# Performance work log

Hardware: AMD Instinct MI355X
Metric: run time of the kernel (lower is better)

## Reference

```python
import jax, jax.numpy as jnp
import numpy as np

DIM = 32
HID = 128          # edge-MLP hidden width
N = 8192           # total nodes
E = 131072         # total edges
B = 64             # number of graphs
NUM_MP = 3
S2S_STEPS = 3


def setup_inputs() -> dict:
    key = jax.random.key(0)
    ks = jax.random.split(key, 24)
    g = lambda k, shape, s=0.05: jax.random.normal(k, shape, dtype=jnp.float32) * s

    inp = {
        "x": jax.random.normal(ks[0], (N, 1), dtype=jnp.float32),
        "edge_attr": jax.random.uniform(ks[1], (E, 2), dtype=jnp.float32),
        # params
        "lin0_w": g(ks[2], (1, DIM)), "lin0_b": g(ks[3], (DIM,)),
        "enn_w1": g(ks[4], (2, HID)), "enn_b1": g(ks[5], (HID,)),
        "enn_w2": g(ks[6], (HID, DIM * DIM)), "enn_b2": g(ks[7], (DIM * DIM,)),
        "root_w": g(ks[8], (DIM, DIM)), "conv_b": g(ks[9], (DIM,)),
        # GRU (gates ordered r,z,n as in torch)
        "gru_wih": g(ks[10], (DIM, 3 * DIM)), "gru_whh": g(ks[11], (DIM, 3 * DIM)),
        "gru_bih": g(ks[12], (3 * DIM,)), "gru_bhh": g(ks[13], (3 * DIM,)),
        # Set2Set LSTM: input 2*DIM, hidden DIM (gates ordered i,f,g,o as in torch)
        "s2s_wih": g(ks[14], (2 * DIM, 4 * DIM)), "s2s_whh": g(ks[15], (DIM, 4 * DIM)),
        "s2s_bih": g(ks[16], (4 * DIM,)), "s2s_bhh": g(ks[17], (4 * DIM,)),
        "lin1_w": g(ks[18], (2 * DIM, DIM)), "lin1_b": g(ks[19], (DIM,)),
        "lin2_w": g(ks[20], (DIM, 1)), "lin2_b": g(ks[21], (1,)),
        # int args
        "edge_index": jax.random.randint(ks[22], (2, E), 0, N, dtype=jnp.int32),
        "batch": jnp.sort(jax.random.randint(ks[23], (N,), 0, B, dtype=jnp.int32)),
    }
    return inp


def _forward(x, edge_attr, lin0_w, lin0_b, enn_w1, enn_b1, enn_w2, enn_b2,
             root_w, conv_b, gru_wih, gru_whh, gru_bih, gru_bhh,
             s2s_wih, s2s_whh, s2s_bih, s2s_bhh, lin1_w, lin1_b, lin2_w, lin2_b,
             edge_index, batch):
    src, dst = edge_index[0], edge_index[1]

    out = jax.nn.relu(x @ lin0_w + lin0_b)          # [N, DIM]
    h = out                                          # GRU hidden state

    # edge-conditioned weights (constant across MP layers -> hoisted)
    ew = jax.nn.relu(edge_attr @ enn_w1 + enn_b1) @ enn_w2 + enn_b2
    W = ew.reshape(E, DIM, DIM)                      # [E, in, out]

    deg = jnp.maximum(jax.ops.segment_sum(jnp.ones((E,), jnp.float32), dst,
                                          num_segments=N), 1.0)[:, None]

    for _ in range(NUM_MP):
        # NNConv: gather -> per-edge small matmul -> scatter-mean, + root + bias
        msg = jnp.einsum('ed,edo->eo', out[src], W)  # [E, DIM]
        agg = jax.ops.segment_sum(msg, dst, num_segments=N) / deg
        m = jax.nn.relu(agg + out @ root_w + conv_b)
        # GRU cell (single step)
        gi = m @ gru_wih + gru_bih
        gh = h @ gru_whh + gru_bhh
        ir, iz, in_ = jnp.split(gi, 3, axis=-1)
        hr, hz, hn = jnp.split(gh, 3, axis=-1)
        r = jax.nn.sigmoid(ir + hr)
        z = jax.nn.sigmoid(iz + hz)
        n = jnp.tanh(in_ + r * hn)
        h = (1.0 - z) * n + z * h
        out = h

    # Set2Set pooling
    qh = jnp.zeros((B, DIM), jnp.float32)
    qc = jnp.zeros((B, DIM), jnp.float32)
    q_star = jnp.zeros((B, 2 * DIM), jnp.float32)
    for _ in range(S2S_STEPS):
        gates = q_star @ s2s_wih + s2s_bih + qh @ s2s_whh + s2s_bhh
        i_, f_, g_, o_ = jnp.split(gates, 4, axis=-1)
        qc = jax.nn.sigmoid(f_) * qc + jax.nn.sigmoid(i_) * jnp.tanh(g_)
        qh = jax.nn.sigmoid(o_) * jnp.tanh(qc)       # [B, DIM]
        e = jnp.sum(out * qh[batch], axis=-1)        # [N] attention logits
        emax = jax.ops.segment_max(e, batch, num_segments=B)
        a = jnp.exp(e - emax[batch])
        a = a / jax.ops.segment_sum(a, batch, num_segments=B)[batch]
        r_read = jax.ops.segment_sum(a[:, None] * out, batch, num_segments=B)
        q_star = jnp.concatenate([qh, r_read], axis=-1)  # [B, 2*DIM]

    y = jax.nn.relu(q_star @ lin1_w + lin1_b) @ lin2_w + lin2_b
    return y.reshape(-1)                              # [B]


def reference(x, edge_attr, lin0_w, lin0_b, enn_w1, enn_b1, enn_w2, enn_b2,
              root_w, conv_b, gru_wih, gru_whh, gru_bih, gru_bhh,
              s2s_wih, s2s_whh, s2s_bih, s2s_bhh, lin1_w, lin1_b, lin2_w, lin2_b,
              edge_index, batch):
    return _forward(x, edge_attr, lin0_w, lin0_b, enn_w1, enn_b1, enn_w2, enn_b2,
                    root_w, conv_b, gru_wih, gru_whh, gru_bih, gru_bhh,
                    s2s_wih, s2s_whh, s2s_bih, s2s_bhh, lin1_w, lin1_b, lin2_w,
                    lin2_b, edge_index, batch)
```

## Files before the change

kernel.cpp:

```cpp
#include <hip/hip_runtime.h>

#define N_NODES 8192
#define N_EDGES 131072
#define NGRAPH  64
#define DIM     32
#define HID     128
#define SROW    34

__device__ __forceinline__ float sigmoidf_(float x) { return 1.0f / (1.0f + expf(-x)); }

__global__ void init_nodes_kernel(const float* __restrict__ x,
                                  const float* __restrict__ w,
                                  const float* __restrict__ b,
                                  float* __restrict__ out) {
  int idx = blockIdx.x * 256 + threadIdx.x;
  if (idx >= N_NODES * DIM) return;
  int n = idx >> 5, d = idx & 31;
  out[idx] = fmaxf(fmaf(x[n], w[d], b[d]), 0.0f);
}

__global__ void hist_kernel(const int* __restrict__ dst, int* __restrict__ counts) {
  int e = blockIdx.x * 256 + threadIdx.x;
  if (e < N_EDGES) atomicAdd(&counts[dst[e]], 1);
}

__global__ void scan_kernel(const int* __restrict__ counts,
                            int* __restrict__ offsets,
                            float* __restrict__ deg_inv) {
  __shared__ int sm[1024];
  int t = threadIdx.x;
  int base = t * 8;
  int loc[8];
  int s = 0;
#pragma unroll
  for (int i = 0; i < 8; ++i) { loc[i] = s; s += counts[base + i]; }
  sm[t] = s;
  __syncthreads();
  for (int off = 1; off < 1024; off <<= 1) {
    int v = (t >= off) ? sm[t - off] : 0;
    __syncthreads();
    sm[t] += v;
    __syncthreads();
  }
  int excl = (t > 0) ? sm[t - 1] : 0;
#pragma unroll
  for (int i = 0; i < 8; ++i) {
    offsets[base + i] = excl + loc[i];
    int c = counts[base + i];
    deg_inv[base + i] = 1.0f / (float)(c > 0 ? c : 1);
  }
  if (t == 1023) offsets[N_NODES] = sm[1023];
}

__global__ void scatter_kernel(const int* __restrict__ ei,
                               const float* __restrict__ ea,
                               const int* __restrict__ offsets,
                               int* __restrict__ cursor,
                               int* __restrict__ csr_src,
                               float2* __restrict__ csr_ea) {
  int e = blockIdx.x * 256 + threadIdx.x;
  if (e >= N_EDGES) return;
  int d = ei[N_EDGES + e];
  int pos = atomicAdd(&cursor[d], 1);
  int slot = offsets[d] + pos;
  csr_src[slot] = ei[e];
  csr_ea[slot] = make_float2(ea[2 * e], ea[2 * e + 1]);
}

__global__ void gstart_kernel(const int* __restrict__ batch, int* __restrict__ gstart) {
  int n = blockIdx.x * 256 + threadIdx.x;
  if (n >= N_NODES) return;
  int b = batch[n];
  if (n == 0) {
    for (int g = 0; g <= b; ++g) gstart[g] = 0;
  } else {
    int bp = batch[n - 1];
    for (int g = bp + 1; g <= b; ++g) gstart[g] = n;
  }
  if (n == N_NODES - 1) {
    for (int g = b + 1; g <= NGRAPH; ++g) gstart[g] = N_NODES;
  }
}

template <int G, int C>
__global__ __launch_bounds__(256) void mp_kernel(
    const float* __restrict__ out_cur, float* __restrict__ out_nxt,
    const int* __restrict__ offsets, const float* __restrict__ deg_inv,
    const int* __restrict__ csr_src, const float2* __restrict__ csr_ea,
    const float* __restrict__ w1, const float* __restrict__ b1,
    const float* __restrict__ w2, const float* __restrict__ b2,
    const float* __restrict__ root_w, const float* __restrict__ conv_b,
    const float* __restrict__ gwih, const float* __restrict__ gwhh,
    const float* __restrict__ gbih, const float* __restrict__ gbhh) {
  __shared__ float S[G * HID * SROW];
  __shared__ float hidb[C * HID];
  __shared__ float osrcb[C * DIM];
  __shared__ float Ob[G * DIM];
  __shared__ float aggb[G * DIM];
  __shared__ float mb[G * DIM];
  __shared__ float hb[G * DIM];
  __shared__ int offs[G + 1];
  __shared__ float dinvb[G];

  const int t = threadIdx.x;
  const int node0 = blockIdx.x * G;

  if (t <= G) offs[t] = offsets[min(node0 + t, N_NODES)];
  if (t < G) dinvb[t] = deg_inv[min(node0 + t, N_NODES - 1)];

  const int kg = t >> 3, dg = t & 7;
  const int k0 = kg * 4, d0 = dg * 4;
  const int ec = t / (256 / C);
  const int sub = t % (256 / C);
  __syncthreads();

  for (int g = 0; g < G; ++g) {
    float acc[4][4];
#pragma unroll
    for (int i = 0; i < 4; ++i)
#pragma unroll
      for (int j = 0; j < 4; ++j) acc[i][j] = 0.0f;
    float oacc = 0.0f;
    const int base = offs[g], end = offs[g + 1];
    for (int c0 = base; c0 < end; c0 += C) {
      const int cnt = min(C, end - c0);
      __syncthreads();
      if (ec < cnt) {
        const int slot = c0 + ec;
        const float2 eav = csr_ea[slot];
        const int sidx = csr_src[slot];
#pragma unroll
        for (int i = 0; i < HID / (256 / C); ++i) {
          const int k = sub * (HID / (256 / C)) + i;
          float v = fmaf(eav.y, w1[HID + k], fmaf(eav.x, w1[k], b1[k]));
          hidb[ec * HID + k] = fmaxf(v, 0.0f);
        }
        const float2 ov = *(const float2*)(out_cur + sidx * DIM + sub * 2);
        *(float2*)(osrcb + ec * DIM + sub * 2) = ov;
      }
      __syncthreads();
      for (int e = 0; e < cnt; ++e) {
        const float4 hv = *(const float4*)(hidb + e * HID + k0);
        const float4 ov = *(const float4*)(osrcb + e * DIM + d0);
        acc[0][0] = fmaf(hv.x, ov.x, acc[0][0]);
        acc[0][1] = fmaf(hv.x, ov.y, acc[0][1]);
        acc[0][2] = fmaf(hv.x, ov.z, acc[0][2]);
        acc[0][3] = fmaf(hv.x, ov.w, acc[0][3]);
        acc[1][0] = fmaf(hv.y, ov.x, acc[1][0]);
        acc[1][1] = fmaf(hv.y, ov.y, acc[1][1]);
        acc[1][2] = fmaf(hv.y, ov.z, acc[1][2]);
        acc[1][3] = fmaf(hv.y, ov.w, acc[1][3]);
        acc[2][0] = fmaf(hv.z, ov.x, acc[2][0]);
        acc[2][1] = fmaf(hv.z, ov.y, acc[2][1]);
        acc[2][2] = fmaf(hv.z, ov.z, acc[2][2]);
        acc[2][3] = fmaf(hv.z, ov.w, acc[2][3]);
        acc[3][0] = fmaf(hv.w, ov.x, acc[3][0]);
        acc[3][1] = fmaf(hv.w, ov.y, acc[3][1]);
        acc[3][2] = fmaf(hv.w, ov.z, acc[3][2]);
        acc[3][3] = fmaf(hv.w, ov.w, acc[3][3]);
        if (t < DIM) oacc += osrcb[e * DIM + t];
      }
    }
    float* Sg = S + g * HID * SROW;
#pragma unroll
    for (int i = 0; i < 4; ++i) {
      *(float2*)(Sg + (k0 + i) * SROW + d0) = make_float2(acc[i][0], acc[i][1]);
      *(float2*)(Sg + (k0 + i) * SROW + d0 + 2) = make_float2(acc[i][2], acc[i][3]);
    }
    if (t < DIM) Ob[g * DIM + t] = oacc;
  }
  __syncthreads();

  {
    const int ks = t >> 3, og = t & 7;
    const int o0 = og * 4;
    float a4[G][4];
#pragma unroll
    for (int g = 0; g < G; ++g)
#pragma unroll
      for (int j = 0; j < 4; ++j) a4[g][j] = 0.0f;
#pragma unroll
    for (int i = 0; i < 4; ++i) {
      const int k = ks * 4 + i;
      const float* w2k = w2 + k * (DIM * DIM);
#pragma unroll
      for (int dv = 0; dv < 8; ++dv) {
        const float4 wq0 = *(const float4*)(w2k + (dv * 4 + 0) * DIM + o0);
        const float4 wq1 = *(const float4*)(w2k + (dv * 4 + 1) * DIM + o0);
        const float4 wq2 = *(const float4*)(w2k + (dv * 4 + 2) * DIM + o0);
        const float4 wq3 = *(const float4*)(w2k + (dv * 4 + 3) * DIM + o0);
#pragma unroll
        for (int g = 0; g < G; ++g) {
          const float* Srow = S + g * HID * SROW + k * SROW + dv * 4;
          const float2 sa = *(const float2*)(Srow);
          const float2 sb = *(const float2*)(Srow + 2);
          a4[g][0] = fmaf(sa.x, wq0.x, fmaf(sa.y, wq1.x, fmaf(sb.x, wq2.x, fmaf(sb.y, wq3.x, a4[g][0]))));
          a4[g][1] = fmaf(sa.x, wq0.y, fmaf(sa.y, wq1.y, fmaf(sb.x, wq2.y, fmaf(sb.y, wq3.y, a4[g][1]))));
          a4[g][2] = fmaf(sa.x, wq0.z, fmaf(sa.y, wq1.z, fmaf(sb.x, wq2.z, fmaf(sb.y, wq3.z, a4[g][2]))));
          a4[g][3] = fmaf(sa.x, wq0.w, fmaf(sa.y, wq1.w, fmaf(sb.x, wq2.w, fmaf(sb.y, wq3.w, a4[g][3]))));
        }
      }
    }
    __syncthreads();
#pragma unroll
    for (int g = 0; g < G; ++g)
#pragma unroll
      for (int j = 0; j < 4; ++j) S[(g * 4 + j) * 256 + t] = a4[g][j];
  }
  __syncthreads();

  if (t < G * DIM) {
    const int g = t >> 5, o = t & 31;
    const int og = o >> 2, j = o & 3;
    float sum = 0.0f;
    for (int ks = 0; ks < 32; ++ks) sum += S[(g * 4 + j) * 256 + ks * 8 + og];
    float ob = 0.0f;
#pragma unroll
    for (int d = 0; d < DIM; ++d) ob = fmaf(Ob[g * DIM + d], b2[d * DIM + o], ob);
    aggb[t] = (sum + ob) * dinvb[g];
  }
  if (t < G * DIM) {
    const int g = t >> 5, o = t & 31;
    const int node = node0 + g;
    hb[t] = (node < N_NODES) ? out_cur[node * DIM + o] : 0.0f;
  }
  __syncthreads();
  if (t < G * DIM) {
    const int g = t >> 5, o = t & 31;
    float rt = conv_b[o];
#pragma unroll
    for (int d = 0; d < DIM; ++d) rt = fmaf(hb[g * DIM + d], root_w[d * DIM + o], rt);
    mb[t] = fmaxf(aggb[t] + rt, 0.0f);
  }
  __syncthreads();
  if (t < G * DIM) {
    const int g = t >> 5, o = t & 31;
    const int node = node0 + g;
    if (node < N_NODES) {
      float gi[3], gh[3];
#pragma unroll
      for (int jj = 0; jj < 3; ++jj) {
        float si = gbih[jj * DIM + o], sh = gbhh[jj * DIM + o];
#pragma unroll
        for (int d = 0; d < DIM; ++d) {
          si = fmaf(mb[g * DIM + d], gwih[d * 3 * DIM + jj * DIM + o], si);
          sh = fmaf(hb[g * DIM + d], gwhh[d * 3 * DIM + jj * DIM + o], sh);
        }
        gi[jj] = si;
        gh[jj] = sh;
      }
      const float r = sigmoidf_(gi[0] + gh[0]);
      const float z = sigmoidf_(gi[1] + gh[1]);
      const float nn = tanhf(fmaf(r, gh[2], gi[2]));
      out_nxt[node * DIM + o] = (1.0f - z) * nn + z * hb[t];
    }
  }
}

__global__ __launch_bounds__(256) void s2s_kernel(
    const float* __restrict__ outf, const int* __restrict__ gstart,
    const float* __restrict__ wih, const float* __restrict__ whh,
    const float* __restrict__ bih, const float* __restrict__ bhh,
    const float* __restrict__ l1w, const float* __restrict__ l1b,
    const float* __restrict__ l2w, const float* __restrict__ l2b,
    float* __restrict__ y) {
  __shared__ float qh[DIM], qc[DIM], qstar[2 * DIM], gates[4 * DIM];
  __shared__ float wsum[4], wmax[4], wr[4][DIM];
  const int b = blockIdx.x, t = threadIdx.x;
  const int gs = gstart[b], ge = gstart[b + 1];
  const int w = t >> 6, lane = t & 63;
  if (t < DIM) { qh[t] = 0.0f; qc[t] = 0.0f; }
  if (t < 2 * DIM) qstar[t] = 0.0f;
  __syncthreads();
  for (int step = 0; step < 3; ++step) {
    if (t < 4 * DIM) {
      float gv = bih[t] + bhh[t];
      for (int i = 0; i < 2 * DIM; ++i) gv = fmaf(qstar[i], wih[i * 4 * DIM + t], gv);
      for (int i = 0; i < DIM; ++i) gv = fmaf(qh[i], whh[i * 4 * DIM + t], gv);
      gates[t] = gv;
    }
    __syncthreads();
    if (t < DIM) {
      const float ig = sigmoidf_(gates[t]);
      const float fg = sigmoidf_(gates[DIM + t]);
      const float gg = tanhf(gates[2 * DIM + t]);
      const float og = sigmoidf_(gates[3 * DIM + t]);
      const float c = fmaf(fg, qc[t], ig * gg);
      qc[t] = c;
      qh[t] = og * tanhf(c);
    }
    __syncthreads();
    float lmax = -INFINITY;
    for (int n = gs + t; n < ge; n += 256) {
      const float* orow = outf + n * DIM;
      float e = 0.0f;
#pragma unroll
      for (int d = 0; d < DIM; ++d) e = fmaf(orow[d], qh[d], e);
      lmax = fmaxf(lmax, e);
    }
#pragma unroll
    for (int off = 32; off > 0; off >>= 1) lmax = fmaxf(lmax, __shfl_xor(lmax, off));
    if (lane == 0) wmax[w] = lmax;
    __syncthreads();
    const float gmax = fmaxf(fmaxf(wmax[0], wmax[1]), fmaxf(wmax[2], wmax[3]));
    float rl[DIM];
#pragma unroll
    for (int d = 0; d < DIM; ++d) rl[d] = 0.0f;
    float lsum = 0.0f;
    for (int n = gs + t; n < ge; n += 256) {
      const float* orow = outf + n * DIM;
      float e = 0.0f;
#pragma unroll
      for (int d = 0; d < DIM; ++d) e = fmaf(orow[d], qh[d], e);
      const float a = expf(e - gmax);
      lsum += a;
#pragma unroll
      for (int d = 0; d < DIM; ++d) rl[d] = fmaf(a, orow[d], rl[d]);
    }
#pragma unroll
    for (int off = 32; off > 0; off >>= 1) {
      lsum += __shfl_xor(lsum, off);
#pragma unroll
      for (int d = 0; d < DIM; ++d) rl[d] += __shfl_xor(rl[d], off);
    }
    __syncthreads();
    if (lane == 0) {
      wsum[w] = lsum;
#pragma unroll
      for (int d = 0; d < DIM; ++d) wr[w][d] = rl[d];
    }
    __syncthreads();
    if (t < DIM) {
      const float stot = wsum[0] + wsum[1] + wsum[2] + wsum[3];
      const float rv = wr[0][t] + wr[1][t] + wr[2][t] + wr[3][t];
      qstar[t] = qh[t];
      qstar[DIM + t] = (stot > 0.0f) ? rv / stot : 0.0f;
    }
    __syncthreads();
  }
  if (t < DIM) {
    float u = l1b[t];
    for (int i = 0; i < 2 * DIM; ++i) u = fmaf(qstar[i], l1w[i * DIM + t], u);
    u = fmaxf(u, 0.0f);
    float v = u * l2w[t];
#pragma unroll
    for (int off = 16; off > 0; off >>= 1) v += __shfl_xor(v, off);
    if (t == 0) y[b] = v + l2b[0];
  }
}

extern "C" void kernel_launch(void* const* d_in, const int* in_sizes, int n_in,
                              void* d_out, int out_size, void* d_ws, size_t ws_size,
                              hipStream_t stream) {
  const float* x        = (const float*)d_in[0];
  const float* ea       = (const float*)d_in[1];
  const float* lin0_w   = (const float*)d_in[2];
  const float* lin0_b   = (const float*)d_in[3];
  const float* enn_w1   = (const float*)d_in[4];
  const float* enn_b1   = (const float*)d_in[5];
  const float* enn_w2   = (const float*)d_in[6];
  const float* enn_b2   = (const float*)d_in[7];
  const float* root_w   = (const float*)d_in[8];
  const float* conv_b   = (const float*)d_in[9];
  const float* gru_wih  = (const float*)d_in[10];
  const float* gru_whh  = (const float*)d_in[11];
  const float* gru_bih  = (const float*)d_in[12];
  const float* gru_bhh  = (const float*)d_in[13];
  const float* s2s_wih  = (const float*)d_in[14];
  const float* s2s_whh  = (const float*)d_in[15];
  const float* s2s_bih  = (const float*)d_in[16];
  const float* s2s_bhh  = (const float*)d_in[17];
  const float* lin1_w   = (const float*)d_in[18];
  const float* lin1_b   = (const float*)d_in[19];
  const float* lin2_w   = (const float*)d_in[20];
  const float* lin2_b   = (const float*)d_in[21];
  const int*   ei       = (const int*)d_in[22];
  const int*   batch    = (const int*)d_in[23];
  float* y = (float*)d_out;

  char* p = (char*)d_ws;
  auto alloc = [&](size_t bytes) -> void* {
    void* r = (void*)p;
    p += (bytes + 255) & ~(size_t)255;
    return r;
  };
  float*  out_a   = (float*)alloc(N_NODES * DIM * 4);
  float*  out_b   = (float*)alloc(N_NODES * DIM * 4);
  int*    counts  = (int*)alloc(N_NODES * 4);
  int*    offsets = (int*)alloc((N_NODES + 1) * 4);
  int*    cursor  = (int*)alloc(N_NODES * 4);
  int*    csr_src = (int*)alloc(N_EDGES * 4);
  float2* csr_ea  = (float2*)alloc(N_EDGES * 8);
  float*  deg_inv = (float*)alloc(N_NODES * 4);
  int*    gstart  = (int*)alloc((NGRAPH + 1) * 4);
  (void)ws_size; (void)n_in; (void)in_sizes; (void)out_size;

  hipMemsetAsync(counts, 0, N_NODES * 4, stream);
  hipMemsetAsync(cursor, 0, N_NODES * 4, stream);

  init_nodes_kernel<<<(N_NODES * DIM) / 256, 256, 0, stream>>>(x, lin0_w, lin0_b, out_a);
  hist_kernel<<<N_EDGES / 256, 256, 0, stream>>>(ei + N_EDGES, counts);
  scan_kernel<<<1, 1024, 0, stream>>>(counts, offsets, deg_inv);
  scatter_kernel<<<N_EDGES / 256, 256, 0, stream>>>(ei, ea, offsets, cursor, csr_src, csr_ea);
  gstart_kernel<<<N_NODES / 256, 256, 0, stream>>>(batch, gstart);

  constexpr int G = 3, C = 16;
  const int mp_blocks = (N_NODES + G - 1) / G;
  mp_kernel<G, C><<<mp_blocks, 256, 0, stream>>>(
      out_a, out_b, offsets, deg_inv, csr_src, csr_ea, enn_w1, enn_b1, enn_w2, enn_b2,
      root_w, conv_b, gru_wih, gru_whh, gru_bih, gru_bhh);
  mp_kernel<G, C><<<mp_blocks, 256, 0, stream>>>(
      out_b, out_a, offsets, deg_inv, csr_src, csr_ea, enn_w1, enn_b1, enn_w2, enn_b2,
      root_w, conv_b, gru_wih, gru_whh, gru_bih, gru_bhh);
  mp_kernel<G, C><<<mp_blocks, 256, 0, stream>>>(
      out_a, out_b, offsets, deg_inv, csr_src, csr_ea, enn_w1, enn_b1, enn_w2, enn_b2,
      root_w, conv_b, gru_wih, gru_whh, gru_bih, gru_bhh);

  s2s_kernel<<<NGRAPH, 256, 0, stream>>>(out_b, gstart, s2s_wih, s2s_whh, s2s_bih, s2s_bhh,
                                         lin1_w, lin1_b, lin2_w, lin2_b, y);
}
```

Before: 501.6 us.

## Split message passing into build, contract, and epilogue kernels via global S buffer

Replaces the fused per-layer message-passing kernel with three kernels. The first builds per-node S = sum(hidden ⊗ x_src) matrices (4096 floats per node) in global memory. The second contracts S against enn_w2 as a 64-node-tiled GEMM with 16 K-slices of partial sums. The third reduces the partials and applies bias, root weight, ReLU and the GRU update. The aim is to amortise w2 loads across 64 nodes instead of 3, at the cost of writing and reading a 128 MB S buffer and 16 MB of partials per layer. It falls back to the old fused kernel when the workspace is too small.

```diff
diff --git a/kernel.cpp b/kernel.cpp
--- a/kernel.cpp
+++ b/kernel.cpp
@@ -5,6 +5,7 @@
 #define NGRAPH  64
 #define DIM     32
 #define HID     128
+#define SKD     4096
 #define SROW    34
 
 __device__ __forceinline__ float sigmoidf_(float x) { return 1.0f / (1.0f + expf(-x)); }
@@ -80,6 +81,219 @@
   if (n == N_NODES - 1) {
     for (int g = b + 1; g <= NGRAPH; ++g) gstart[g] = N_NODES;
   }
+}
+
+__global__ __launch_bounds__(256) void build_s_kernel(
+    const float* __restrict__ out_cur, const int* __restrict__ offsets,
+    const int* __restrict__ csr_src, const float2* __restrict__ csr_ea,
+    const float* __restrict__ w1, const float* __restrict__ b1,
+    float* __restrict__ S, float* __restrict__ O) {
+  constexpr int C = 16;
+  __shared__ float hidb[C * HID];
+  __shared__ float osrcb[C * DIM];
+  __shared__ int offs[5];
+  const int t = threadIdx.x;
+  const int node0 = blockIdx.x * 4;
+  if (t <= 4) offs[t] = offsets[node0 + t];
+  const int k0 = (t >> 3) * 4, d0 = (t & 7) * 4;
+  const int ec = t >> 4;
+  const int sub = t & 15;
+  float acc[4][4][4];
+#pragma unroll
+  for (int g = 0; g < 4; ++g)
+#pragma unroll
+    for (int i = 0; i < 4; ++i)
+#pragma unroll
+      for (int j = 0; j < 4; ++j) acc[g][i][j] = 0.0f;
+  float oacc[4] = {0.0f, 0.0f, 0.0f, 0.0f};
+  __syncthreads();
+#pragma unroll
+  for (int g = 0; g < 4; ++g) {
+    const int base = offs[g], end = offs[g + 1];
+    for (int c0 = base; c0 < end; c0 += C) {
+      const int cnt = min(C, end - c0);
+      __syncthreads();
+      if (ec < cnt) {
+        const int slot = c0 + ec;
+        const float2 eav = csr_ea[slot];
+        const int sidx = csr_src[slot];
+#pragma unroll
+        for (int i = 0; i < 8; ++i) {
+          const int k = sub * 8 + i;
+          hidb[ec * HID + k] =
+              fmaxf(fmaf(eav.y, w1[HID + k], fmaf(eav.x, w1[k], b1[k])), 0.0f);
+        }
+        *(float2*)(osrcb + ec * DIM + sub * 2) =
+            *(const float2*)(out_cur + sidx * DIM + sub * 2);
+      }
+      __syncthreads();
+      for (int e = 0; e < cnt; ++e) {
+        const float4 hv = *(const float4*)(hidb + e * HID + k0);
+        const float4 ov = *(const float4*)(osrcb + e * DIM + d0);
+        acc[g][0][0] = fmaf(hv.x, ov.x, acc[g][0][0]);
+        acc[g][0][1] = fmaf(hv.x, ov.y, acc[g][0][1]);
+        acc[g][0][2] = fmaf(hv.x, ov.z, acc[g][0][2]);
+        acc[g][0][3] = fmaf(hv.x, ov.w, acc[g][0][3]);
+        acc[g][1][0] = fmaf(hv.y, ov.x, acc[g][1][0]);
+        acc[g][1][1] = fmaf(hv.y, ov.y, acc[g][1][1]);
+        acc[g][1][2] = fmaf(hv.y, ov.z, acc[g][1][2]);
+        acc[g][1][3] = fmaf(hv.y, ov.w, acc[g][1][3]);
+        acc[g][2][0] = fmaf(hv.z, ov.x, acc[g][2][0]);
+        acc[g][2][1] = fmaf(hv.z, ov.y, acc[g][2][1]);
+        acc[g][2][2] = fmaf(hv.z, ov.z, acc[g][2][2]);
+        acc[g][2][3] = fmaf(hv.z, ov.w, acc[g][2][3]);
+        acc[g][3][0] = fmaf(hv.w, ov.x, acc[g][3][0]);
+        acc[g][3][1] = fmaf(hv.w, ov.y, acc[g][3][1]);
+        acc[g][3][2] = fmaf(hv.w, ov.z, acc[g][3][2]);
+        acc[g][3][3] = fmaf(hv.w, ov.w, acc[g][3][3]);
+        if (t < DIM) oacc[g] += osrcb[e * DIM + t];
+      }
+    }
+  }
+#pragma unroll
+  for (int g = 0; g < 4; ++g) {
+    const int node = node0 + g;
+    float* Sp = S + node * SKD + k0 * DIM + d0;
+#pragma unroll
+    for (int i = 0; i < 4; ++i)
+      *(float4*)(Sp + i * DIM) =
+          make_float4(acc[g][i][0], acc[g][i][1], acc[g][i][2], acc[g][i][3]);
+    if (t < DIM) O[node * DIM + t] = oacc[g];
+  }
+}
+
+#define SBPAD 68
+__global__ __launch_bounds__(256) void contract_kernel(
+    const float* __restrict__ S, const float* __restrict__ w2,
+    float* __restrict__ partial) {
+  __shared__ float sb[64 * SBPAD];
+  const int t = threadIdx.x;
+  const int nb = blockIdx.x >> 2;
+  const int kqb = blockIdx.x & 3;
+  const int node0 = nb * 64;
+  const int kbase = kqb * 1024;
+  const int w = t >> 6;
+  const int lane = t & 63;
+  const int ng = (lane >> 3) & 7;
+  const int og = lane & 7;
+  const int o0 = og * 4;
+  float acc[8][4];
+#pragma unroll
+  for (int i = 0; i < 8; ++i)
+#pragma unroll
+    for (int j = 0; j < 4; ++j) acc[i][j] = 0.0f;
+
+  const int ld_node = t >> 2;
+  const int ld_kds = (t & 3) * 16;
+
+  for (int c = 0; c < 16; ++c) {
+    __syncthreads();
+    const float* gsrc = S + (size_t)(node0 + ld_node) * SKD + kbase + c * 64 + ld_kds;
+#pragma unroll
+    for (int i = 0; i < 4; ++i) {
+      const float4 v = *(const float4*)(gsrc + i * 4);
+      const int kl = ld_kds + i * 4;
+      sb[(kl + 0) * SBPAD + ld_node] = v.x;
+      sb[(kl + 1) * SBPAD + ld_node] = v.y;
+      sb[(kl + 2) * SBPAD + ld_node] = v.z;
+      sb[(kl + 3) * SBPAD + ld_node] = v.w;
+    }
+    __syncthreads();
+#pragma unroll
+    for (int k4 = 0; k4 < 4; ++k4) {
+#pragma unroll
+      for (int kk = 0; kk < 4; ++kk) {
+        const int kdl = w * 16 + k4 * 4 + kk;
+        const int kd = kbase + c * 64 + kdl;
+        const float4 wv = *(const float4*)(w2 + (size_t)kd * 32 + o0);
+        const float4 sa = *(const float4*)(sb + kdl * SBPAD + ng * 8);
+        const float4 sc = *(const float4*)(sb + kdl * SBPAD + ng * 8 + 4);
+        acc[0][0] = fmaf(sa.x, wv.x, acc[0][0]);
+        acc[0][1] = fmaf(sa.x, wv.y, acc[0][1]);
+        acc[0][2] = fmaf(sa.x, wv.z, acc[0][2]);
+        acc[0][3] = fmaf(sa.x, wv.w, acc[0][3]);
+        acc[1][0] = fmaf(sa.y, wv.x, acc[1][0]);
+        acc[1][1] = fmaf(sa.y, wv.y, acc[1][1]);
+        acc[1][2] = fmaf(sa.y, wv.z, acc[1][2]);
+        acc[1][3] = fmaf(sa.y, wv.w, acc[1][3]);
+        acc[2][0] = fmaf(sa.z, wv.x, acc[2][0]);
+        acc[2][1] = fmaf(sa.z, wv.y, acc[2][1]);
+        acc[2][2] = fmaf(sa.z, wv.z, acc[2][2]);
+        acc[2][3] = fmaf(sa.z, wv.w, acc[2][3]);
+        acc[3][0] = fmaf(sa.w, wv.x, acc[3][0]);
+        acc[3][1] = fmaf(sa.w, wv.y, acc[3][1]);
+        acc[3][2] = fmaf(sa.w, wv.z, acc[3][2]);
+        acc[3][3] = fmaf(sa.w, wv.w, acc[3][3]);
+        acc[4][0] = fmaf(sc.x, wv.x, acc[4][0]);
+        acc[4][1] = fmaf(sc.x, wv.y, acc[4][1]);
+        acc[4][2] = fmaf(sc.x, wv.z, acc[4][2]);
+        acc[4][3] = fmaf(sc.x, wv.w, acc[4][3]);
+        acc[5][0] = fmaf(sc.y, wv.x, acc[5][0]);
+        acc[5][1] = fmaf(sc.y, wv.y, acc[5][1]);
+        acc[5][2] = fmaf(sc.y, wv.z, acc[5][2]);
+        acc[5][3] = fmaf(sc.y, wv.w, acc[5][3]);
+        acc[6][0] = fmaf(sc.z, wv.x, acc[6][0]);
+        acc[6][1] = fmaf(sc.z, wv.y, acc[6][1]);
+        acc[6][2] = fmaf(sc.z, wv.z, acc[6][2]);
+        acc[6][3] = fmaf(sc.z, wv.w, acc[6][3]);
+        acc[7][0] = fmaf(sc.w, wv.x, acc[7][0]);
+        acc[7][1] = fmaf(sc.w, wv.y, acc[7][1]);
+        acc[7][2] = fmaf(sc.w, wv.z, acc[7][2]);
+        acc[7][3] = fmaf(sc.w, wv.w, acc[7][3]);
+      }
+    }
+  }
+  const int slice = kqb * 4 + w;
+  float* pp = partial + ((size_t)slice * N_NODES + node0 + ng * 8) * DIM + o0;
+#pragma unroll
+  for (int i = 0; i < 8; ++i)
+    *(float4*)(pp + i * DIM) = make_float4(acc[i][0], acc[i][1], acc[i][2], acc[i][3]);
+}
+
+__global__ __launch_bounds__(256) void epilogue_kernel(
+    const float* __restrict__ partial, const float* __restrict__ O,
+    const float* __restrict__ out_cur, const float* __restrict__ b2,
+    const float* __restrict__ deg_inv, const float* __restrict__ root_w,
+    const float* __restrict__ conv_b, const float* __restrict__ gwih,
+    const float* __restrict__ gwhh, const float* __restrict__ gbih,
+    const float* __restrict__ gbhh, float* __restrict__ out_nxt) {
+  __shared__ float hb[256], ob[256], mb[256], b2s[1024];
+  const int t = threadIdx.x;
+  const int node0 = blockIdx.x * 8;
+  hb[t] = out_cur[node0 * DIM + t];
+  ob[t] = O[node0 * DIM + t];
+#pragma unroll
+  for (int i = 0; i < 4; ++i) b2s[i * 256 + t] = b2[i * 256 + t];
+  __syncthreads();
+  const int g = t >> 5, o = t & 31;
+  const int node = node0 + g;
+  float agg = 0.0f;
+#pragma unroll
+  for (int s = 0; s < 16; ++s) agg += partial[(size_t)s * N_NODES * DIM + node * DIM + o];
+#pragma unroll
+  for (int d = 0; d < DIM; ++d) agg = fmaf(ob[g * DIM + d], b2s[d * DIM + o], agg);
+  agg *= deg_inv[node];
+  float rt = conv_b[o];
+#pragma unroll
+  for (int d = 0; d < DIM; ++d) rt = fmaf(hb[g * DIM + d], root_w[d * DIM + o], rt);
+  mb[t] = fmaxf(agg + rt, 0.0f);
+  __syncthreads();
+  float gi[3], gh[3];
+#pragma unroll
+  for (int jj = 0; jj < 3; ++jj) {
+    float si = gbih[jj * DIM + o], sh = gbhh[jj * DIM + o];
+#pragma unroll
+    for (int d = 0; d < DIM; ++d) {
+      si = fmaf(mb[g * DIM + d], gwih[d * 3 * DIM + jj * DIM + o], si);
+      sh = fmaf(hb[g * DIM + d], gwhh[d * 3 * DIM + jj * DIM + o], sh);
+    }
+    gi[jj] = si;
+    gh[jj] = sh;
+  }
+  const float r = sigmoidf_(gi[0] + gh[0]);
+  const float z = sigmoidf_(gi[1] + gh[1]);
+  const float nn = tanhf(fmaf(r, gh[2], gi[2]));
+  out_nxt[node * DIM + o] = (1.0f - z) * nn + z * hb[t];
 }
 
 template <int G, int C>
@@ -101,19 +315,15 @@
   __shared__ float hb[G * DIM];
   __shared__ int offs[G + 1];
   __shared__ float dinvb[G];
-
   const int t = threadIdx.x;
   const int node0 = blockIdx.x * G;
-
   if (t <= G) offs[t] = offsets[min(node0 + t, N_NODES)];
   if (t < G) dinvb[t] = deg_inv[min(node0 + t, N_NODES - 1)];
-
   const int kg = t >> 3, dg = t & 7;
   const int k0 = kg * 4, d0 = dg * 4;
   const int ec = t / (256 / C);
   const int sub = t % (256 / C);
   __syncthreads();
-
   for (int g = 0; g < G; ++g) {
     float acc[4][4];
 #pragma unroll
@@ -135,8 +345,8 @@
           float v = fmaf(eav.y, w1[HID + k], fmaf(eav.x, w1[k], b1[k]));
           hidb[ec * HID + k] = fmaxf(v, 0.0f);
         }
-        const float2 ov = *(const float2*)(out_cur + sidx * DIM + sub * 2);
-        *(float2*)(osrcb + ec * DIM + sub * 2) = ov;
+        const float2 ovv = *(const float2*)(out_cur + sidx * DIM + sub * 2);
+        *(float2*)(osrcb + ec * DIM + sub * 2) = ovv;
       }
       __syncthreads();
       for (int e = 0; e < cnt; ++e) {
@@ -170,7 +380,6 @@
     if (t < DIM) Ob[g * DIM + t] = oacc;
   }
   __syncthreads();
-
   {
     const int ks = t >> 3, og = t & 7;
     const int o0 = og * 4;
@@ -193,11 +402,11 @@
         for (int g = 0; g < G; ++g) {
           const float* Srow = S + g * HID * SROW + k * SROW + dv * 4;
           const float2 sa = *(const float2*)(Srow);
-          const float2 sb = *(const float2*)(Srow + 2);
-          a4[g][0] = fmaf(sa.x, wq0.x, fmaf(sa.y, wq1.x, fmaf(sb.x, wq2.x, fmaf(sb.y, wq3.x, a4[g][0]))));
-          a4[g][1] = fmaf(sa.x, wq0.y, fmaf(sa.y, wq1.y, fmaf(sb.x, wq2.y, fmaf(sb.y, wq3.y, a4[g][1]))));
-          a4[g][2] = fmaf(sa.x, wq0.z, fmaf(sa.y, wq1.z, fmaf(sb.x, wq2.z, fmaf(sb.y, wq3.z, a4[g][2]))));
-          a4[g][3] = fmaf(sa.x, wq0.w, fmaf(sa.y, wq1.w, fmaf(sb.x, wq2.w, fmaf(sb.y, wq3.w, a4[g][3]))));
+          const float2 sbv = *(const float2*)(Srow + 2);
+          a4[g][0] = fmaf(sa.x, wq0.x, fmaf(sa.y, wq1.x, fmaf(sbv.x, wq2.x, fmaf(sbv.y, wq3.x, a4[g][0]))));
+          a4[g][1] = fmaf(sa.x, wq0.y, fmaf(sa.y, wq1.y, fmaf(sbv.x, wq2.y, fmaf(sbv.y, wq3.y, a4[g][1]))));
+          a4[g][2] = fmaf(sa.x, wq0.z, fmaf(sa.y, wq1.z, fmaf(sbv.x, wq2.z, fmaf(sbv.y, wq3.z, a4[g][2]))));
+          a4[g][3] = fmaf(sa.x, wq0.w, fmaf(sa.y, wq1.w, fmaf(sbv.x, wq2.w, fmaf(sbv.y, wq3.w, a4[g][3]))));
         }
       }
     }
@@ -208,16 +417,15 @@
       for (int j = 0; j < 4; ++j) S[(g * 4 + j) * 256 + t] = a4[g][j];
   }
   __syncthreads();
-
   if (t < G * DIM) {
     const int g = t >> 5, o = t & 31;
     const int og = o >> 2, j = o & 3;
     float sum = 0.0f;
     for (int ks = 0; ks < 32; ++ks) sum += S[(g * 4 + j) * 256 + ks * 8 + og];
-    float ob = 0.0f;
-#pragma unroll
-    for (int d = 0; d < DIM; ++d) ob = fmaf(Ob[g * DIM + d], b2[d * DIM + o], ob);
-    aggb[t] = (sum + ob) * dinvb[g];
+    float obv = 0.0f;
+#pragma unroll
+    for (int d = 0; d < DIM; ++d) obv = fmaf(Ob[g * DIM + d], b2[d * DIM + o], obv);
+    aggb[t] = (sum + obv) * dinvb[g];
   }
   if (t < G * DIM) {
     const int g = t >> 5, o = t & 31;
@@ -393,7 +601,12 @@
   float2* csr_ea  = (float2*)alloc(N_EDGES * 8);
   float*  deg_inv = (float*)alloc(N_NODES * 4);
   int*    gstart  = (int*)alloc((NGRAPH + 1) * 4);
-  (void)ws_size; (void)n_in; (void)in_sizes; (void)out_size;
+  float*  Sbuf    = (float*)alloc((size_t)N_NODES * SKD * 4);
+  float*  Obuf    = (float*)alloc((size_t)N_NODES * DIM * 4);
+  float*  partial = (float*)alloc((size_t)16 * N_NODES * DIM * 4);
+  const size_t need = (size_t)(p - (char*)d_ws);
+  const bool big = (ws_size >= need);
+  (void)n_in; (void)in_sizes; (void)out_size;
 
   hipMemsetAsync(counts, 0, N_NODES * 4, stream);
   hipMemsetAsync(cursor, 0, N_NODES * 4, stream);
@@ -404,18 +617,33 @@
   scatter_kernel<<<N_EDGES / 256, 256, 0, stream>>>(ei, ea, offsets, cursor, csr_src, csr_ea);
   gstart_kernel<<<N_NODES / 256, 256, 0, stream>>>(batch, gstart);
 
-  constexpr int G = 3, C = 16;
-  const int mp_blocks = (N_NODES + G - 1) / G;
-  mp_kernel<G, C><<<mp_blocks, 256, 0, stream>>>(
-      out_a, out_b, offsets, deg_inv, csr_src, csr_ea, enn_w1, enn_b1, enn_w2, enn_b2,
-      root_w, conv_b, gru_wih, gru_whh, gru_bih, gru_bhh);
-  mp_kernel<G, C><<<mp_blocks, 256, 0, stream>>>(
-      out_b, out_a, offsets, deg_inv, csr_src, csr_ea, enn_w1, enn_b1, enn_w2, enn_b2,
-      root_w, conv_b, gru_wih, gru_whh, gru_bih, gru_bhh);
-  mp_kernel<G, C><<<mp_blocks, 256, 0, stream>>>(
-      out_a, out_b, offsets, deg_inv, csr_src, csr_ea, enn_w1, enn_b1, enn_w2, enn_b2,
-      root_w, conv_b, gru_wih, gru_whh, gru_bih, gru_bhh);
-
-  s2s_kernel<<<NGRAPH, 256, 0, stream>>>(out_b, gstart, s2s_wih, s2s_whh, s2s_bih, s2s_bhh,
-                                         lin1_w, lin1_b, lin2_w, lin2_b, y);
-}
+  if (big) {
+    const float* cur = out_a;
+    float* nxt = out_b;
+    for (int layer = 0; layer < 3; ++layer) {
+      build_s_kernel<<<N_NODES / 4, 256, 0, stream>>>(
+          cur, offsets, csr_src, csr_ea, enn_w1, enn_b1, Sbuf, Obuf);
+      contract_kernel<<<(N_NODES / 64) * 4, 256, 0, stream>>>(Sbuf, enn_w2, partial);
+      epilogue_kernel<<<N_NODES / 8, 256, 0, stream>>>(
+          partial, Obuf, cur, enn_b2, deg_inv, root_w, conv_b,
+          gru_wih, gru_whh, gru_bih, gru_bhh, nxt);
+      const float* tmp = cur; cur = nxt; nxt = (float*)tmp;
+    }
+    s2s_kernel<<<NGRAPH, 256, 0, stream>>>(cur, gstart, s2s_wih, s2s_whh, s2s_bih,
+                                           s2s_bhh, lin1_w, lin1_b, lin2_w, lin2_b, y);
+  } else {
+    constexpr int G = 3, C = 16;
+    const int mp_blocks = (N_NODES + G - 1) / G;
+    mp_kernel<G, C><<<mp_blocks, 256, 0, stream>>>(
+        out_a, out_b, offsets, deg_inv, csr_src, csr_ea, enn_w1, enn_b1, enn_w2,
+        enn_b2, root_w, conv_b, gru_wih, gru_whh, gru_bih, gru_bhh);
+    mp_kernel<G, C><<<mp_blocks, 256, 0, stream>>>(
+        out_b, out_a, offsets, deg_inv, csr_src, csr_ea, enn_w1, enn_b1, enn_w2,
+        enn_b2, root_w, conv_b, gru_wih, gru_whh, gru_bih, gru_bhh);
+    mp_kernel<G, C><<<mp_blocks, 256, 0, stream>>>(
+        out_a, out_b, offsets, deg_inv, csr_src, csr_ea, enn_w1, enn_b1, enn_w2,
+        enn_b2, root_w, conv_b, gru_wih, gru_whh, gru_bih, gru_bhh);
+    s2s_kernel<<<NGRAPH, 256, 0, stream>>>(out_b, gstart, s2s_wih, s2s_whh, s2s_bih,
+                                           s2s_bhh, lin1_w, lin1_b, lin2_w, lin2_b, y);
+  }
+}
```

After: 635.8 us. 1.27x slower.

## Split message-passing across hidden halves, move GRU epilogue to separate kernel

Applied to the files above, without the earlier changes.

The per-layer message-passing kernel is split so that each node group is handled by two blocks, each covering half of the 128-wide edge-MLP hidden dimension. Each block writes a partial aggregate to a global buffer, and a new epilogue kernel sums the halves and applies the bias term, root weight and GRU update. The goal is twice the block count and a smaller shared-memory footprint (with a launch-bounds occupancy hint) so more blocks stay resident. In exchange it adds global partial-sum traffic and an extra launch per layer. The small preprocessing kernels are also merged pairwise to cut launch count.

```diff
diff --git a/kernel.cpp b/kernel.cpp
--- a/kernel.cpp
+++ b/kernel.cpp
@@ -5,23 +5,24 @@
 #define NGRAPH  64
 #define DIM     32
 #define HID     128
+#define KHALF   64
+#define G_NODES 3
 #define SROW    34
 
 __device__ __forceinline__ float sigmoidf_(float x) { return 1.0f / (1.0f + expf(-x)); }
 
-__global__ void init_nodes_kernel(const float* __restrict__ x,
-                                  const float* __restrict__ w,
-                                  const float* __restrict__ b,
-                                  float* __restrict__ out) {
-  int idx = blockIdx.x * 256 + threadIdx.x;
-  if (idx >= N_NODES * DIM) return;
-  int n = idx >> 5, d = idx & 31;
-  out[idx] = fmaxf(fmaf(x[n], w[d], b[d]), 0.0f);
-}
-
-__global__ void hist_kernel(const int* __restrict__ dst, int* __restrict__ counts) {
-  int e = blockIdx.x * 256 + threadIdx.x;
-  if (e < N_EDGES) atomicAdd(&counts[dst[e]], 1);
+__global__ void prep1_kernel(const float* __restrict__ x, const float* __restrict__ w,
+                             const float* __restrict__ b, float* __restrict__ out,
+                             const int* __restrict__ dst, int* __restrict__ counts) {
+  const int bb = blockIdx.x;
+  if (bb < 1024) {
+    int idx = bb * 256 + threadIdx.x;
+    int n = idx >> 5, d = idx & 31;
+    out[idx] = fmaxf(fmaf(x[n], w[d], b[d]), 0.0f);
+  } else {
+    int e = (bb - 1024) * 256 + threadIdx.x;
+    atomicAdd(&counts[dst[e]], 1);
+  }
 }
 
 __global__ void scan_kernel(const int* __restrict__ counts,
@@ -52,75 +53,68 @@
   if (t == 1023) offsets[N_NODES] = sm[1023];
 }
 
-__global__ void scatter_kernel(const int* __restrict__ ei,
-                               const float* __restrict__ ea,
-                               const int* __restrict__ offsets,
-                               int* __restrict__ cursor,
-                               int* __restrict__ csr_src,
-                               float2* __restrict__ csr_ea) {
-  int e = blockIdx.x * 256 + threadIdx.x;
-  if (e >= N_EDGES) return;
-  int d = ei[N_EDGES + e];
-  int pos = atomicAdd(&cursor[d], 1);
-  int slot = offsets[d] + pos;
-  csr_src[slot] = ei[e];
-  csr_ea[slot] = make_float2(ea[2 * e], ea[2 * e + 1]);
-}
-
-__global__ void gstart_kernel(const int* __restrict__ batch, int* __restrict__ gstart) {
-  int n = blockIdx.x * 256 + threadIdx.x;
-  if (n >= N_NODES) return;
-  int b = batch[n];
-  if (n == 0) {
-    for (int g = 0; g <= b; ++g) gstart[g] = 0;
+__global__ void prep2_kernel(const int* __restrict__ ei, const float* __restrict__ ea,
+                             const int* __restrict__ offsets, int* __restrict__ cursor,
+                             int* __restrict__ csr_src, float2* __restrict__ csr_ea,
+                             const int* __restrict__ batch, int* __restrict__ gstart) {
+  const int bb = blockIdx.x;
+  if (bb < 512) {
+    int e = bb * 256 + threadIdx.x;
+    int d = ei[N_EDGES + e];
+    int pos = atomicAdd(&cursor[d], 1);
+    int slot = offsets[d] + pos;
+    csr_src[slot] = ei[e];
+    csr_ea[slot] = make_float2(ea[2 * e], ea[2 * e + 1]);
   } else {
-    int bp = batch[n - 1];
-    for (int g = bp + 1; g <= b; ++g) gstart[g] = n;
-  }
-  if (n == N_NODES - 1) {
-    for (int g = b + 1; g <= NGRAPH; ++g) gstart[g] = N_NODES;
-  }
-}
-
-template <int G, int C>
-__global__ __launch_bounds__(256) void mp_kernel(
-    const float* __restrict__ out_cur, float* __restrict__ out_nxt,
-    const int* __restrict__ offsets, const float* __restrict__ deg_inv,
+    int n = (bb - 512) * 256 + threadIdx.x;
+    int b = batch[n];
+    if (n == 0) {
+      for (int g = 0; g <= b; ++g) gstart[g] = 0;
+    } else {
+      int bp = batch[n - 1];
+      for (int g = bp + 1; g <= b; ++g) gstart[g] = n;
+    }
+    if (n == N_NODES - 1) {
+      for (int g = b + 1; g <= NGRAPH; ++g) gstart[g] = N_NODES;
+    }
+  }
+}
+
+__global__ __launch_bounds__(256, 4) void mp_half_kernel(
+    const float* __restrict__ out_cur, const int* __restrict__ offsets,
     const int* __restrict__ csr_src, const float2* __restrict__ csr_ea,
     const float* __restrict__ w1, const float* __restrict__ b1,
-    const float* __restrict__ w2, const float* __restrict__ b2,
-    const float* __restrict__ root_w, const float* __restrict__ conv_b,
-    const float* __restrict__ gwih, const float* __restrict__ gwhh,
-    const float* __restrict__ gbih, const float* __restrict__ gbhh) {
-  __shared__ float S[G * HID * SROW];
-  __shared__ float hidb[C * HID];
-  __shared__ float osrcb[C * DIM];
-  __shared__ float Ob[G * DIM];
-  __shared__ float aggb[G * DIM];
-  __shared__ float mb[G * DIM];
-  __shared__ float hb[G * DIM];
-  __shared__ int offs[G + 1];
-  __shared__ float dinvb[G];
+    const float* __restrict__ w2, float* __restrict__ partial,
+    float* __restrict__ O) {
+  constexpr int C = 16;
+  __shared__ float smem[G_NODES * KHALF * SROW + C * KHALF + C * DIM];
+  float* S = smem;
+  float* hidb = smem + G_NODES * KHALF * SROW;
+  float* osrcb = hidb + C * KHALF;
+  float* red = smem;
+  __shared__ int offs[G_NODES + 1];
 
   const int t = threadIdx.x;
-  const int node0 = blockIdx.x * G;
-
-  if (t <= G) offs[t] = offsets[min(node0 + t, N_NODES)];
-  if (t < G) dinvb[t] = deg_inv[min(node0 + t, N_NODES - 1)];
-
-  const int kg = t >> 3, dg = t & 7;
-  const int k0 = kg * 4, d0 = dg * 4;
-  const int ec = t / (256 / C);
-  const int sub = t % (256 / C);
-  __syncthreads();
-
-  for (int g = 0; g < G; ++g) {
-    float acc[4][4];
-#pragma unroll
-    for (int i = 0; i < 4; ++i)
-#pragma unroll
-      for (int j = 0; j < 4; ++j) acc[i][j] = 0.0f;
-    float oacc = 0.0f;
+  const int bb = blockIdx.x;
+  const int khalf = bb & 1;
+  const int node0 = (bb >> 1) * G_NODES;
+
+  if (t <= G_NODES) offs[t] = offsets[min(node0 + t, N_NODES)];
+
+  const int kg = t >> 4, dg = t & 15;
+  const int k0 = kg * 4, d0 = dg * 2;
+  const int ec = t >> 4, sub = t & 15;
+
+  float acc[G_NODES][4][2];
+#pragma unroll
+  for (int g = 0; g < G_NODES; ++g)
+#pragma unroll
+    for (int i = 0; i < 4; ++i) { acc[g][i][0] = 0.0f; acc[g][i][1] = 0.0f; }
+  float oacc[G_NODES] = {0.0f, 0.0f, 0.0f};
+  __syncthreads();
+
+#pragma unroll
+  for (int g = 0; g < G_NODES; ++g) {
     const int base = offs[g], end = offs[g + 1];
     for (int c0 = base; c0 < end; c0 += C) {
       const int cnt = min(C, end - c0);
@@ -130,131 +124,141 @@
         const float2 eav = csr_ea[slot];
         const int sidx = csr_src[slot];
 #pragma unroll
-        for (int i = 0; i < HID / (256 / C); ++i) {
-          const int k = sub * (HID / (256 / C)) + i;
-          float v = fmaf(eav.y, w1[HID + k], fmaf(eav.x, w1[k], b1[k]));
-          hidb[ec * HID + k] = fmaxf(v, 0.0f);
+        for (int i = 0; i < 4; ++i) {
+          const int kl = sub * 4 + i;
+          const int kgl = khalf * KHALF + kl;
+          hidb[ec * KHALF + kl] =
+              fmaxf(fmaf(eav.y, w1[HID + kgl], fmaf(eav.x, w1[kgl], b1[kgl])), 0.0f);
         }
-        const float2 ov = *(const float2*)(out_cur + sidx * DIM + sub * 2);
-        *(float2*)(osrcb + ec * DIM + sub * 2) = ov;
+        *(float2*)(osrcb + ec * DIM + sub * 2) =
+            *(const float2*)(out_cur + sidx * DIM + sub * 2);
       }
       __syncthreads();
       for (int e = 0; e < cnt; ++e) {
-        const float4 hv = *(const float4*)(hidb + e * HID + k0);
-        const float4 ov = *(const float4*)(osrcb + e * DIM + d0);
-        acc[0][0] = fmaf(hv.x, ov.x, acc[0][0]);
-        acc[0][1] = fmaf(hv.x, ov.y, acc[0][1]);
-        acc[0][2] = fmaf(hv.x, ov.z, acc[0][2]);
-        acc[0][3] = fmaf(hv.x, ov.w, acc[0][3]);
-        acc[1][0] = fmaf(hv.y, ov.x, acc[1][0]);
-        acc[1][1] = fmaf(hv.y, ov.y, acc[1][1]);
-        acc[1][2] = fmaf(hv.y, ov.z, acc[1][2]);
-        acc[1][3] = fmaf(hv.y, ov.w, acc[1][3]);
-        acc[2][0] = fmaf(hv.z, ov.x, acc[2][0]);
-        acc[2][1] = fmaf(hv.z, ov.y, acc[2][1]);
-        acc[2][2] = fmaf(hv.z, ov.z, acc[2][2]);
-        acc[2][3] = fmaf(hv.z, ov.w, acc[2][3]);
-        acc[3][0] = fmaf(hv.w, ov.x, acc[3][0]);
-        acc[3][1] = fmaf(hv.w, ov.y, acc[3][1]);
-        acc[3][2] = fmaf(hv.w, ov.z, acc[3][2]);
-        acc[3][3] = fmaf(hv.w, ov.w, acc[3][3]);
-        if (t < DIM) oacc += osrcb[e * DIM + t];
+        const float4 hv = *(const float4*)(hidb + e * KHALF + k0);
+        const float2 ov = *(const float2*)(osrcb + e * DIM + d0);
+        acc[g][0][0] = fmaf(hv.x, ov.x, acc[g][0][0]);
+        acc[g][0][1] = fmaf(hv.x, ov.y, acc[g][0][1]);
+        acc[g][1][0] = fmaf(hv.y, ov.x, acc[g][1][0]);
+        acc[g][1][1] = fmaf(hv.y, ov.y, acc[g][1][1]);
+        acc[g][2][0] = fmaf(hv.z, ov.x, acc[g][2][0]);
+        acc[g][2][1] = fmaf(hv.z, ov.y, acc[g][2][1]);
+        acc[g][3][0] = fmaf(hv.w, ov.x, acc[g][3][0]);
+        acc[g][3][1] = fmaf(hv.w, ov.y, acc[g][3][1]);
+        if (khalf == 0 && t < DIM) oacc[g] += osrcb[e * DIM + t];
       }
     }
-    float* Sg = S + g * HID * SROW;
+  }
+#pragma unroll
+  for (int g = 0; g < G_NODES; ++g) {
+    float* Sg = S + g * KHALF * SROW;
+#pragma unroll
+    for (int i = 0; i < 4; ++i)
+      *(float2*)(Sg + (k0 + i) * SROW + d0) = make_float2(acc[g][i][0], acc[g][i][1]);
+  }
+  if (khalf == 0 && t < DIM) {
+#pragma unroll
+    for (int g = 0; g < G_NODES; ++g) {
+      const int node = node0 + g;
+      if (node < N_NODES) O[node * DIM + t] = oacc[g];
+    }
+  }
+  __syncthreads();
+
+  {
+    const int ks = t >> 4;
+    const int dvh = (t >> 3) & 1;
+    const int og = t & 7;
+    float a4[G_NODES][4];
+#pragma unroll
+    for (int g = 0; g < G_NODES; ++g)
+#pragma unroll
+      for (int r = 0; r < 4; ++r) a4[g][r] = 0.0f;
 #pragma unroll
     for (int i = 0; i < 4; ++i) {
-      *(float2*)(Sg + (k0 + i) * SROW + d0) = make_float2(acc[i][0], acc[i][1]);
-      *(float2*)(Sg + (k0 + i) * SROW + d0 + 2) = make_float2(acc[i][2], acc[i][3]);
-    }
-    if (t < DIM) Ob[g * DIM + t] = oacc;
-  }
-  __syncthreads();
-
-  {
-    const int ks = t >> 3, og = t & 7;
-    const int o0 = og * 4;
-    float a4[G][4];
-#pragma unroll
-    for (int g = 0; g < G; ++g)
-#pragma unroll
-      for (int j = 0; j < 4; ++j) a4[g][j] = 0.0f;
-#pragma unroll
-    for (int i = 0; i < 4; ++i) {
-      const int k = ks * 4 + i;
-      const float* w2k = w2 + k * (DIM * DIM);
-#pragma unroll
-      for (int dv = 0; dv < 8; ++dv) {
-        const float4 wq0 = *(const float4*)(w2k + (dv * 4 + 0) * DIM + o0);
-        const float4 wq1 = *(const float4*)(w2k + (dv * 4 + 1) * DIM + o0);
-        const float4 wq2 = *(const float4*)(w2k + (dv * 4 + 2) * DIM + o0);
-        const float4 wq3 = *(const float4*)(w2k + (dv * 4 + 3) * DIM + o0);
-#pragma unroll
-        for (int g = 0; g < G; ++g) {
-          const float* Srow = S + g * HID * SROW + k * SROW + dv * 4;
-          const float2 sa = *(const float2*)(Srow);
-          const float2 sb = *(const float2*)(Srow + 2);
-          a4[g][0] = fmaf(sa.x, wq0.x, fmaf(sa.y, wq1.x, fmaf(sb.x, wq2.x, fmaf(sb.y, wq3.x, a4[g][0]))));
-          a4[g][1] = fmaf(sa.x, wq0.y, fmaf(sa.y, wq1.y, fmaf(sb.x, wq2.y, fmaf(sb.y, wq3.y, a4[g][1]))));
-          a4[g][2] = fmaf(sa.x, wq0.z, fmaf(sa.y, wq1.z, fmaf(sb.x, wq2.z, fmaf(sb.y, wq3.z, a4[g][2]))));
-          a4[g][3] = fmaf(sa.x, wq0.w, fmaf(sa.y, wq1.w, fmaf(sb.x, wq2.w, fmaf(sb.y, wq3.w, a4[g][3]))));
+      const int kl = ks * 4 + i;
+      const float* w2k = w2 + (size_t)(khalf * KHALF + kl) * (DIM * DIM);
+#pragma unroll
+      for (int dvi = 0; dvi < 4; ++dvi) {
+        const int dv = dvh * 4 + dvi;
+#pragma unroll
+        for (int r = 0; r < 4; ++r) {
+          const int d = dv * 4 + r;
+          const float4 wv = *(const float4*)(w2k + d * DIM + og * 4);
+#pragma unroll
+          for (int g = 0; g < G_NODES; ++g) {
+            const float sv = S[g * KHALF * SROW + kl * SROW + d];
+            a4[g][0] = fmaf(sv, wv.x, a4[g][0]);
+            a4[g][1] = fmaf(sv, wv.y, a4[g][1]);
+            a4[g][2] = fmaf(sv, wv.z, a4[g][2]);
+            a4[g][3] = fmaf(sv, wv.w, a4[g][3]);
+          }
         }
       }
     }
     __syncthreads();
 #pragma unroll
-    for (int g = 0; g < G; ++g)
-#pragma unroll
-      for (int j = 0; j < 4; ++j) S[(g * 4 + j) * 256 + t] = a4[g][j];
-  }
-  __syncthreads();
-
-  if (t < G * DIM) {
+    for (int g = 0; g < G_NODES; ++g)
+#pragma unroll
+      for (int r = 0; r < 4; ++r) red[(g * 4 + r) * 256 + t] = a4[g][r];
+  }
+  __syncthreads();
+  if (t < G_NODES * DIM) {
     const int g = t >> 5, o = t & 31;
-    const int og = o >> 2, j = o & 3;
+    const int og = o >> 2, r = o & 3;
+    const float* rp = red + (g * 4 + r) * 256 + og;
     float sum = 0.0f;
-    for (int ks = 0; ks < 32; ++ks) sum += S[(g * 4 + j) * 256 + ks * 8 + og];
-    float ob = 0.0f;
-#pragma unroll
-    for (int d = 0; d < DIM; ++d) ob = fmaf(Ob[g * DIM + d], b2[d * DIM + o], ob);
-    aggb[t] = (sum + ob) * dinvb[g];
-  }
-  if (t < G * DIM) {
-    const int g = t >> 5, o = t & 31;
+#pragma unroll
+    for (int j = 0; j < 32; ++j) sum += rp[j * 8];
     const int node = node0 + g;
-    hb[t] = (node < N_NODES) ? out_cur[node * DIM + o] : 0.0f;
-  }
-  __syncthreads();
-  if (t < G * DIM) {
-    const int g = t >> 5, o = t & 31;
-    float rt = conv_b[o];
-#pragma unroll
-    for (int d = 0; d < DIM; ++d) rt = fmaf(hb[g * DIM + d], root_w[d * DIM + o], rt);
-    mb[t] = fmaxf(aggb[t] + rt, 0.0f);
-  }
-  __syncthreads();
-  if (t < G * DIM) {
-    const int g = t >> 5, o = t & 31;
-    const int node = node0 + g;
-    if (node < N_NODES) {
-      float gi[3], gh[3];
-#pragma unroll
-      for (int jj = 0; jj < 3; ++jj) {
-        float si = gbih[jj * DIM + o], sh = gbhh[jj * DIM + o];
-#pragma unroll
-        for (int d = 0; d < DIM; ++d) {
-          si = fmaf(mb[g * DIM + d], gwih[d * 3 * DIM + jj * DIM + o], si);
-          sh = fmaf(hb[g * DIM + d], gwhh[d * 3 * DIM + jj * DIM + o], sh);
-        }
-        gi[jj] = si;
-        gh[jj] = sh;
-      }
-      const float r = sigmoidf_(gi[0] + gh[0]);
-      const float z = sigmoidf_(gi[1] + gh[1]);
-      const float nn = tanhf(fmaf(r, gh[2], gi[2]));
-      out_nxt[node * DIM + o] = (1.0f - z) * nn + z * hb[t];
-    }
-  }
+    if (node < N_NODES)
+      partial[(size_t)khalf * N_NODES * DIM + node * DIM + o] = sum;
+  }
+}
+
+__global__ __launch_bounds__(256) void epilogue_kernel(
+    const float* __restrict__ partial, const float* __restrict__ O,
+    const float* __restrict__ out_cur, const float* __restrict__ b2,
+    const float* __restrict__ deg_inv, const float* __restrict__ root_w,
+    const float* __restrict__ conv_b, const float* __restrict__ gwih,
+    const float* __restrict__ gwhh, const float* __restrict__ gbih,
+    const float* __restrict__ gbhh, float* __restrict__ out_nxt) {
+  __shared__ float hb[256], ob[256], mb[256], b2s[1024];
+  const int t = threadIdx.x;
+  const int node0 = blockIdx.x * 8;
+  hb[t] = out_cur[node0 * DIM + t];
+  ob[t] = O[node0 * DIM + t];
+#pragma unroll
+  for (int i = 0; i < 4; ++i) b2s[i * 256 + t] = b2[i * 256 + t];
+  __syncthreads();
+  const int g = t >> 5, o = t & 31;
+  const int node = node0 + g;
+  float agg = partial[node * DIM + o] +
+              partial[(size_t)N_NODES * DIM + node * DIM + o];
+#pragma unroll
+  for (int d = 0; d < DIM; ++d) agg = fmaf(ob[g * DIM + d], b2s[d * DIM + o], agg);
+  agg *= deg_inv[node];
+  float rt = conv_b[o];
+#pragma unroll
+  for (int d = 0; d < DIM; ++d) rt = fmaf(hb[g * DIM + d], root_w[d * DIM + o], rt);
+  mb[t] = fmaxf(agg + rt, 0.0f);
+  __syncthreads();
+  float gi[3], gh[3];
+#pragma unroll
+  for (int jj = 0; jj < 3; ++jj) {
+    float si = gbih[jj * DIM + o], sh = gbhh[jj * DIM + o];
+#pragma unroll
+    for (int d = 0; d < DIM; ++d) {
+      si = fmaf(mb[g * DIM + d], gwih[d * 3 * DIM + jj * DIM + o], si);
+      sh = fmaf(hb[g * DIM + d], gwhh[d * 3 * DIM + jj * DIM + o], sh);
+    }
+    gi[jj] = si;
+    gh[jj] = sh;
+  }
+  const float r = sigmoidf_(gi[0] + gh[0]);
+  const float z = sigmoidf_(gi[1] + gh[1]);
+  const float nn = tanhf(fmaf(r, gh[2], gi[2]));
+  out_nxt[node * DIM + o] = (1.0f - z) * nn + z * hb[t];
 }
 
 __global__ __launch_bounds__(256) void s2s_kernel(
@@ -393,29 +397,31 @@
   float2* csr_ea  = (float2*)alloc(N_EDGES * 8);
   float*  deg_inv = (float*)alloc(N_NODES * 4);
   int*    gstart  = (int*)alloc((NGRAPH + 1) * 4);
+  float*  Obuf    = (float*)alloc((size_t)N_NODES * DIM * 4);
+  float*  partial = (float*)alloc((size_t)2 * N_NODES * DIM * 4);
   (void)ws_size; (void)n_in; (void)in_sizes; (void)out_size;
 
   hipMemsetAsync(counts, 0, N_NODES * 4, stream);
   hipMemsetAsync(cursor, 0, N_NODES * 4, stream);
 
-  init_nodes_kernel<<<(N_NODES * DIM) / 256, 256, 0, stream>>>(x, lin0_w, lin0_b, out_a);
-  hist_kernel<<<N_EDGES / 256, 256, 0, stream>>>(ei + N_EDGES, counts);
+  prep1_kernel<<<1024 + 512, 256, 0, stream>>>(x, lin0_w, lin0_b, out_a,
+                                               ei + N_EDGES, counts);
   scan_kernel<<<1, 1024, 0, stream>>>(counts, offsets, deg_inv);
-  scatter_kernel<<<N_EDGES / 256, 256, 0, stream>>>(ei, ea, offsets, cursor, csr_src, csr_ea);
-  gstart_kernel<<<N_NODES / 256, 256, 0, stream>>>(batch, gstart);
-
-  constexpr int G = 3, C = 16;
-  const int mp_blocks = (N_NODES + G - 1) / G;
-  mp_kernel<G, C><<<mp_blocks, 256, 0, stream>>>(
-      out_a, out_b, offsets, deg_inv, csr_src, csr_ea, enn_w1, enn_b1, enn_w2, enn_b2,
-      root_w, conv_b, gru_wih, gru_whh, gru_bih, gru_bhh);
-  mp_kernel<G, C><<<mp_blocks, 256, 0, stream>>>(
-      out_b, out_a, offsets, deg_inv, csr_src, csr_ea, enn_w1, enn_b1, enn_w2, enn_b2,
-      root_w, conv_b, gru_wih, gru_whh, gru_bih, gru_bhh);
-  mp_kernel<G, C><<<mp_blocks, 256, 0, stream>>>(
-      out_a, out_b, offsets, deg_inv, csr_src, csr_ea, enn_w1, enn_b1, enn_w2, enn_b2,
-      root_w, conv_b, gru_wih, gru_whh, gru_bih, gru_bhh);
-
-  s2s_kernel<<<NGRAPH, 256, 0, stream>>>(out_b, gstart, s2s_wih, s2s_whh, s2s_bih, s2s_bhh,
-                                         lin1_w, lin1_b, lin2_w, lin2_b, y);
-}
+  prep2_kernel<<<512 + 32, 256, 0, stream>>>(ei, ea, offsets, cursor, csr_src,
+                                             csr_ea, batch, gstart);
+
+  const int ngroups = (N_NODES + G_NODES - 1) / G_NODES;
+  const float* cur = out_a;
+  float* nxt = out_b;
+  for (int layer = 0; layer < 3; ++layer) {
+    mp_half_kernel<<<ngroups * 2, 256, 0, stream>>>(
+        cur, offsets, csr_src, csr_ea, enn_w1, enn_b1, enn_w2, partial, Obuf);
+    epilogue_kernel<<<N_NODES / 8, 256, 0, stream>>>(
+        partial, Obuf, cur, enn_b2, deg_inv, root_w, conv_b,
+        gru_wih, gru_whh, gru_bih, gru_bhh, nxt);
+    const float* tmp = cur; cur = nxt; nxt = (float*)tmp;
+  }
+
+  s2s_kernel<<<NGRAPH, 256, 0, stream>>>(cur, gstart, s2s_wih, s2s_whh, s2s_bih,
+                                         s2s_bhh, lin1_w, lin1_b, lin2_w, lin2_b, y);
+}
```

After: 455.1 us. 1.1x faster.
